# Optimization experiments

Measured on AMD Instinct MI355X. Metric: run time of the kernel, lower is better.

Reference implementation:

```python
import jax, jax.numpy as jnp
import numpy as np

B, C, H, W = 32, 256, 64, 64
K = 32

def setup_inputs() -> dict:
    key = jax.random.key(0)
    k1, k2, k3 = jax.random.split(key, 3)
    x = jax.random.normal(k1, (B, C, H, W), dtype=jnp.float32)
    codewords = jax.random.normal(k2, (K, C), dtype=jnp.float32)
    scale = jax.random.normal(k3, (K,), dtype=jnp.float32)
    return {"x": x, "codewords": codewords, "scale": scale}

def reference(x, codewords, scale):
    Bb, Cc, Hh, Ww = x.shape
    # features: [B, N, C] with N = H*W
    features = x.reshape(Bb, Cc, Hh * Ww).transpose(0, 2, 1)
    # Euclidean cdist via ||f||^2 + ||c||^2 - 2 f.c  -> [B, N, K]
    f2 = jnp.sum(features * features, axis=-1, keepdims=True)       # [B,N,1]
    c2 = jnp.sum(codewords * codewords, axis=-1)                     # [K]
    fc = jnp.einsum('bnc,kc->bnk', features, codewords)              # [B,N,K]
    dist = jnp.sqrt(jnp.maximum(f2 + c2[None, None, :] - 2.0 * fc, 0.0))
    # softmax over codewords with per-code scale
    assignment = jax.nn.softmax(-dist * scale[None, None, :], axis=2)  # [B,N,K]
    # encoded[b,k,c] = sum_n a[b,n,k] * (f[b,n,c] - cw[k,c])
    # factored to avoid materializing the [B,N,K,C] residual tensor
    enc = jnp.einsum('bnk,bnc->bkc', assignment, features)
    a_sum = jnp.sum(assignment, axis=1)                              # [B,K]
    encoded = enc - a_sum[:, :, None] * codewords[None, :, :]        # [B,K,C]
    return encoded.mean(axis=1)                                      # [B,C]
```

## Files before the change

### kernel.cpp

```cpp
#include <hip/hip_runtime.h>
#include <hip/hip_bf16.h>
#include <math.h>

#define B_DIM 32
#define C_DIM 256
#define K_DIM 32
#define N_DIM 4096
#define NSLICE 16
#define RS 66

typedef short v8s __attribute__((ext_vector_type(8)));
typedef float v4f __attribute__((ext_vector_type(4)));

#define WS_SPART 0
#define WS_APART 131072

__device__ __forceinline__ unsigned pack_bf16(float lo, float hi) {
    union { __hip_bfloat16 h; unsigned short u; } a, b;
    a.h = __float2bfloat16(lo);
    b.h = __float2bfloat16(hi);
    return ((unsigned)b.u << 16) | a.u;
}

__global__ __launch_bounds__(256, 2)
void ce_main(const float* __restrict__ x,
             const float* __restrict__ cw,
             const float* __restrict__ scale,
             float* __restrict__ Spart,
             float* __restrict__ a_part) {
    __shared__ float buf[2][4][16 * RS];
    __shared__ unsigned cwl[K_DIM][132];
    __shared__ float sA[4][C_DIM];
    __shared__ float awv[4][K_DIM];
    __shared__ float f2s[4][64];
    __shared__ float csl[64];

    const int tid   = threadIdx.x;
    const int wave  = tid >> 6;
    const int lane  = tid & 63;
    const int g     = lane >> 4;
    const int m     = lane & 15;
    const int ig    = lane >> 4;
    const int q     = lane & 15;
    const int slice = blockIdx.x;
    const int b     = blockIdx.y;

    const float* xw = x + (size_t)b * C_DIM * N_DIM + slice * 256 + wave * 64;

    float4 xv[8];
    #pragma unroll
    for (int j = 0; j < 4; ++j)
        #pragma unroll
        for (int r = 0; r < 2; ++r)
            xv[2 * j + r] = *(const float4*)(xw + (size_t)(2 * (4 * ig + j) + r) * N_DIM + 4 * q);

    {
        const int r = tid >> 3, c8 = tid & 7;
        float4 cv[8];
        #pragma unroll
        for (int j = 0; j < 8; ++j)
            cv[j] = ((const float4*)(cw + (size_t)r * C_DIM + c8 * 32))[j];
        float sq = 0.f;
        #pragma unroll
        for (int j = 0; j < 8; ++j) {
            sq = fmaf(cv[j].x, cv[j].x, sq);
            sq = fmaf(cv[j].y, cv[j].y, sq);
            sq = fmaf(cv[j].z, cv[j].z, sq);
            sq = fmaf(cv[j].w, cv[j].w, sq);
        }
        sq += __shfl_xor(sq, 1);
        sq += __shfl_xor(sq, 2);
        sq += __shfl_xor(sq, 4);
        if (c8 == 0) csl[r] = sq;
        if (tid < K_DIM) csl[32 + tid] = scale[tid];
        #pragma unroll
        for (int w = 0; w < 4; ++w) {
            uint4 o;
            o.x = pack_bf16(cv[2 * w].x, cv[2 * w].y);
            o.y = pack_bf16(cv[2 * w].z, cv[2 * w].w);
            o.z = pack_bf16(cv[2 * w + 1].x, cv[2 * w + 1].y);
            o.w = pack_bf16(cv[2 * w + 1].z, cv[2 * w + 1].w);
            *(uint4*)&cwl[r][16 * c8 + 4 * w] = o;
        }
    }
    __syncthreads();

    uint4 afr[2][8];
    #pragma unroll
    for (int u = 0; u < 2; ++u)
        #pragma unroll
        for (int s = 0; s < 8; ++s)
            afr[u][s] = ((const uint4*)&cwl[16 * u + m][0])[4 * s + g];

    float* b0 = &buf[0][wave][0];
    float* b1 = &buf[1][wave][0];

    v4f acc[2][4];
    #pragma unroll
    for (int u = 0; u < 2; ++u)
        #pragma unroll
        for (int t = 0; t < 4; ++t) acc[u][t] = (v4f){0.f, 0.f, 0.f, 0.f};

    float f2q[4] = {0.f, 0.f, 0.f, 0.f};
    float sLo[8], sHi[8];

    #pragma unroll
    for (int j = 0; j < 4; ++j) {
        float4 r0 = xv[2 * j], r1 = xv[2 * j + 1];
        f2q[0] = fmaf(r0.x, r0.x, f2q[0]); f2q[0] = fmaf(r1.x, r1.x, f2q[0]);
        f2q[1] = fmaf(r0.y, r0.y, f2q[1]); f2q[1] = fmaf(r1.y, r1.y, f2q[1]);
        f2q[2] = fmaf(r0.z, r0.z, f2q[2]); f2q[2] = fmaf(r1.z, r1.z, f2q[2]);
        f2q[3] = fmaf(r0.w, r0.w, f2q[3]); f2q[3] = fmaf(r1.w, r1.w, f2q[3]);
        unsigned* dst = &((unsigned*)b0)[(4 * ig + j) * RS + 4 * q];
        dst[0] = pack_bf16(r0.x, r1.x);
        dst[1] = pack_bf16(r0.y, r1.y);
        dst[2] = pack_bf16(r0.z, r1.z);
        dst[3] = pack_bf16(r0.w, r1.w);
    }

    #pragma unroll
    for (int s = 0; s < 8; ++s) {
        float* cb = (s & 1) ? b1 : b0;
        float* nb = (s & 1) ? b0 : b1;

        if (s < 7) {
            #pragma unroll
            for (int j = 0; j < 4; ++j)
                #pragma unroll
                for (int r = 0; r < 2; ++r)
                    xv[2 * j + r] = *(const float4*)(xw +
                        (size_t)(32 * (s + 1) + 2 * (4 * ig + j) + r) * N_DIM + 4 * q);
        }

        #pragma unroll
        for (int t = 0; t < 4; ++t) {
            union { unsigned d[4]; v8s v; } fb;
            #pragma unroll
            for (int h = 0; h < 4; ++h)
                fb.d[h] = ((const unsigned*)cb)[(4 * g + h) * RS + 16 * t + m];
            union { uint4 u; v8s v; } a0, a1;
            a0.u = afr[0][s]; a1.u = afr[1][s];
            acc[0][t] = __builtin_amdgcn_mfma_f32_16x16x32_bf16(a0.v, fb.v, acc[0][t], 0, 0, 0);
            acc[1][t] = __builtin_amdgcn_mfma_f32_16x16x32_bf16(a1.v, fb.v, acc[1][t], 0, 0, 0);
        }

        {
            float aLo = 0.f, aHi = 0.f;
            #pragma unroll
            for (int qq = 0; qq < 8; ++qq) {
                uint2 w = ((const uint2*)cb)[33 * m + 8 * g + qq];
                aLo += __uint_as_float(w.x << 16) + __uint_as_float(w.y << 16);
                aHi += __uint_as_float(w.x & 0xffff0000u) + __uint_as_float(w.y & 0xffff0000u);
            }
            aLo += __shfl_xor(aLo, 16); aLo += __shfl_xor(aLo, 32);
            aHi += __shfl_xor(aHi, 16); aHi += __shfl_xor(aHi, 32);
            sLo[s] = aLo; sHi[s] = aHi;
        }

        if (s < 7) {
            #pragma unroll
            for (int j = 0; j < 4; ++j) {
                float4 r0 = xv[2 * j], r1 = xv[2 * j + 1];
                f2q[0] = fmaf(r0.x, r0.x, f2q[0]); f2q[0] = fmaf(r1.x, r1.x, f2q[0]);
                f2q[1] = fmaf(r0.y, r0.y, f2q[1]); f2q[1] = fmaf(r1.y, r1.y, f2q[1]);
                f2q[2] = fmaf(r0.z, r0.z, f2q[2]); f2q[2] = fmaf(r1.z, r1.z, f2q[2]);
                f2q[3] = fmaf(r0.w, r0.w, f2q[3]); f2q[3] = fmaf(r1.w, r1.w, f2q[3]);
                unsigned* dst = &((unsigned*)nb)[(4 * ig + j) * RS + 4 * q];
                dst[0] = pack_bf16(r0.x, r1.x);
                dst[1] = pack_bf16(r0.y, r1.y);
                dst[2] = pack_bf16(r0.z, r1.z);
                dst[3] = pack_bf16(r0.w, r1.w);
            }
        }
    }

    #pragma unroll
    for (int p = 0; p < 4; ++p) {
        f2q[p] += __shfl_xor(f2q[p], 16);
        f2q[p] += __shfl_xor(f2q[p], 32);
    }
    if (lane < 16) {
        f2s[wave][4 * q + 0] = f2q[0];
        f2s[wave][4 * q + 1] = f2q[1];
        f2s[wave][4 * q + 2] = f2q[2];
        f2s[wave][4 * q + 3] = f2q[3];
    }

    float c2v[2][4], scv[2][4];
    #pragma unroll
    for (int u = 0; u < 2; ++u)
        #pragma unroll
        for (int r = 0; r < 4; ++r) {
            int k = 16 * u + 4 * g + r;
            c2v[u][r] = csl[k];
            scv[u][r] = csl[32 + k];
        }

    float aacc[2][4] = {{0.f,0.f,0.f,0.f},{0.f,0.f,0.f,0.f}};
    #pragma unroll
    for (int t = 0; t < 4; ++t) {
        float f2t = f2s[wave][16 * t + m];
        float L[2][4];
        float mx = -1e30f;
        #pragma unroll
        for (int u = 0; u < 2; ++u)
            #pragma unroll
            for (int r = 0; r < 4; ++r) {
                float d2 = f2t + c2v[u][r] - 2.f * acc[u][t][r];
                float dist = sqrtf(fmaxf(d2, 0.f));
                float Lv = -dist * scv[u][r];
                L[u][r] = Lv;
                mx = fmaxf(mx, Lv);
            }
        mx = fmaxf(mx, __shfl_xor(mx, 16));
        mx = fmaxf(mx, __shfl_xor(mx, 32));
        float e[2][4], ss = 0.f;
        #pragma unroll
        for (int u = 0; u < 2; ++u)
            #pragma unroll
            for (int r = 0; r < 4; ++r) {
                e[u][r] = __expf(L[u][r] - mx);
                ss += e[u][r];
            }
        ss += __shfl_xor(ss, 16);
        ss += __shfl_xor(ss, 32);
        float inv = 1.f / ss;
        #pragma unroll
        for (int u = 0; u < 2; ++u)
            #pragma unroll
            for (int r = 0; r < 4; ++r)
                aacc[u][r] = fmaf(e[u][r], inv, aacc[u][r]);
    }

    #pragma unroll
    for (int u = 0; u < 2; ++u)
        #pragma unroll
        for (int r = 0; r < 4; ++r) {
            float v = aacc[u][r];
            v += __shfl_xor(v, 1);
            v += __shfl_xor(v, 2);
            v += __shfl_xor(v, 4);
            v += __shfl_xor(v, 8);
            if (m == 0) awv[wave][16 * u + 4 * g + r] = v;
        }

    if (g == 0) {
        #pragma unroll
        for (int s = 0; s < 8; ++s) {
            sA[wave][32 * s + 2 * m]     = sLo[s];
            sA[wave][32 * s + 2 * m + 1] = sHi[s];
        }
    }
    __syncthreads();

    float Ssum = sA[0][tid] + sA[1][tid] + sA[2][tid] + sA[3][tid];
    Spart[((size_t)b * NSLICE + slice) * C_DIM + tid] = Ssum;
    if (tid < K_DIM)
        a_part[((size_t)b * NSLICE + slice) * K_DIM + tid] =
            awv[0][tid] + awv[1][tid] + awv[2][tid] + awv[3][tid];
}

__global__ void ce_final(float* __restrict__ out,
                         const float* __restrict__ cw,
                         const float* __restrict__ Spart,
                         const float* __restrict__ a_part) {
    __shared__ float asum[K_DIM];
    const int b = blockIdx.x;
    const int c = threadIdx.x;

    if (c < K_DIM) {
        float a = 0.f;
        #pragma unroll
        for (int s = 0; s < NSLICE; ++s)
            a += a_part[((size_t)b * NSLICE + s) * K_DIM + c];
        asum[c] = a;
    }
    __syncthreads();

    float S = 0.f;
    #pragma unroll
    for (int s = 0; s < NSLICE; ++s)
        S += Spart[((size_t)b * NSLICE + s) * C_DIM + c];

    float acc2 = 0.f;
    #pragma unroll
    for (int k = 0; k < K_DIM; ++k)
        acc2 = fmaf(asum[k], cw[k * C_DIM + c], acc2);
    out[b * C_DIM + c] = (S - acc2) * (1.0f / (float)K_DIM);
}

extern "C" void kernel_launch(void* const* d_in, const int* in_sizes, int n_in,
                              void* d_out, int out_size, void* d_ws, size_t ws_size,
                              hipStream_t stream) {
    const float* x     = (const float*)d_in[0];
    const float* cw    = (const float*)d_in[1];
    const float* scale = (const float*)d_in[2];
    float* out = (float*)d_out;
    float* ws  = (float*)d_ws;

    dim3 grid(NSLICE, B_DIM);
    ce_main<<<grid, 256, 0, stream>>>(x, cw, scale,
                                      ws + WS_SPART, ws + WS_APART);

    ce_final<<<B_DIM, 256, 0, stream>>>(out, cw,
                                        ws + WS_SPART, ws + WS_APART);
}
```

Baseline: 40.65 us.

## Split each block's pixels across eight waves and compute channel sums in fp32

Doubles the threads per block from 256 to 512 so each wave handles 32 pixels instead of 64, which halves per-thread registers and global loads. Codeword MFMA fragments are now loaded from LDS on every step rather than held in registers for the whole loop. Per-channel sums are computed from the fp32 values during packing with shuffle reductions, replacing the separate pass that read the bf16 LDS tile back. The intent is more resident waves to hide memory latency, at the cost of more LDS traffic and more cross-wave reduction work.

```diff
diff --git a/kernel.cpp b/kernel.cpp
--- a/kernel.cpp
+++ b/kernel.cpp
@@ -7,7 +7,7 @@
 #define K_DIM 32
 #define N_DIM 4096
 #define NSLICE 16
-#define RS 66
+#define RSD 34
 
 typedef short v8s __attribute__((ext_vector_type(8)));
 typedef float v4f __attribute__((ext_vector_type(4)));
@@ -22,17 +22,17 @@
     return ((unsigned)b.u << 16) | a.u;
 }
 
-__global__ __launch_bounds__(256, 2)
+__global__ __launch_bounds__(512, 4)
 void ce_main(const float* __restrict__ x,
              const float* __restrict__ cw,
              const float* __restrict__ scale,
              float* __restrict__ Spart,
              float* __restrict__ a_part) {
-    __shared__ float buf[2][4][16 * RS];
+    __shared__ float buf[2][8][16 * RSD];
     __shared__ unsigned cwl[K_DIM][132];
-    __shared__ float sA[4][C_DIM];
-    __shared__ float awv[4][K_DIM];
-    __shared__ float f2s[4][64];
+    __shared__ float sA[8][C_DIM];
+    __shared__ float awv[8][K_DIM];
+    __shared__ float f2s[8][32];
     __shared__ float csl[64];
 
     const int tid   = threadIdx.x;
@@ -40,29 +40,29 @@
     const int lane  = tid & 63;
     const int g     = lane >> 4;
     const int m     = lane & 15;
-    const int ig    = lane >> 4;
-    const int q     = lane & 15;
+    const int r0    = lane >> 3;
+    const int qd    = lane & 7;
     const int slice = blockIdx.x;
     const int b     = blockIdx.y;
 
-    const float* xw = x + (size_t)b * C_DIM * N_DIM + slice * 256 + wave * 64;
-
-    float4 xv[8];
-    #pragma unroll
-    for (int j = 0; j < 4; ++j)
-        #pragma unroll
-        for (int r = 0; r < 2; ++r)
-            xv[2 * j + r] = *(const float4*)(xw + (size_t)(2 * (4 * ig + j) + r) * N_DIM + 4 * q);
+    const float* xw = x + (size_t)b * C_DIM * N_DIM + slice * 256 + wave * 32;
+
+    float4 xv[4];
+    #pragma unroll
+    for (int j = 0; j < 2; ++j)
+        #pragma unroll
+        for (int rr = 0; rr < 2; ++rr)
+            xv[2 * j + rr] = *(const float4*)(xw + (size_t)(2 * (r0 + 8 * j) + rr) * N_DIM + 4 * qd);
 
     {
-        const int r = tid >> 3, c8 = tid & 7;
-        float4 cv[8];
-        #pragma unroll
-        for (int j = 0; j < 8; ++j)
-            cv[j] = ((const float4*)(cw + (size_t)r * C_DIM + c8 * 32))[j];
+        const int r = tid >> 4, c16 = tid & 15;
+        float4 cv[4];
+        #pragma unroll
+        for (int j = 0; j < 4; ++j)
+            cv[j] = ((const float4*)(cw + (size_t)r * C_DIM + c16 * 16))[j];
         float sq = 0.f;
         #pragma unroll
-        for (int j = 0; j < 8; ++j) {
+        for (int j = 0; j < 4; ++j) {
             sq = fmaf(cv[j].x, cv[j].x, sq);
             sq = fmaf(cv[j].y, cv[j].y, sq);
             sq = fmaf(cv[j].z, cv[j].z, sq);
@@ -71,52 +71,63 @@
         sq += __shfl_xor(sq, 1);
         sq += __shfl_xor(sq, 2);
         sq += __shfl_xor(sq, 4);
-        if (c8 == 0) csl[r] = sq;
+        sq += __shfl_xor(sq, 8);
+        if (c16 == 0) csl[r] = sq;
         if (tid < K_DIM) csl[32 + tid] = scale[tid];
-        #pragma unroll
-        for (int w = 0; w < 4; ++w) {
-            uint4 o;
-            o.x = pack_bf16(cv[2 * w].x, cv[2 * w].y);
-            o.y = pack_bf16(cv[2 * w].z, cv[2 * w].w);
-            o.z = pack_bf16(cv[2 * w + 1].x, cv[2 * w + 1].y);
-            o.w = pack_bf16(cv[2 * w + 1].z, cv[2 * w + 1].w);
-            *(uint4*)&cwl[r][16 * c8 + 4 * w] = o;
-        }
+        uint4 o0, o1;
+        o0.x = pack_bf16(cv[0].x, cv[0].y); o0.y = pack_bf16(cv[0].z, cv[0].w);
+        o0.z = pack_bf16(cv[1].x, cv[1].y); o0.w = pack_bf16(cv[1].z, cv[1].w);
+        o1.x = pack_bf16(cv[2].x, cv[2].y); o1.y = pack_bf16(cv[2].z, cv[2].w);
+        o1.z = pack_bf16(cv[3].x, cv[3].y); o1.w = pack_bf16(cv[3].z, cv[3].w);
+        *(uint4*)&cwl[r][8 * c16]     = o0;
+        *(uint4*)&cwl[r][8 * c16 + 4] = o1;
     }
     __syncthreads();
-
-    uint4 afr[2][8];
-    #pragma unroll
-    for (int u = 0; u < 2; ++u)
-        #pragma unroll
-        for (int s = 0; s < 8; ++s)
-            afr[u][s] = ((const uint4*)&cwl[16 * u + m][0])[4 * s + g];
 
     float* b0 = &buf[0][wave][0];
     float* b1 = &buf[1][wave][0];
 
-    v4f acc[2][4];
+    v4f acc[2][2];
     #pragma unroll
     for (int u = 0; u < 2; ++u)
         #pragma unroll
-        for (int t = 0; t < 4; ++t) acc[u][t] = (v4f){0.f, 0.f, 0.f, 0.f};
+        for (int t = 0; t < 2; ++t) acc[u][t] = (v4f){0.f, 0.f, 0.f, 0.f};
 
     float f2q[4] = {0.f, 0.f, 0.f, 0.f};
-    float sLo[8], sHi[8];
-
-    #pragma unroll
-    for (int j = 0; j < 4; ++j) {
-        float4 r0 = xv[2 * j], r1 = xv[2 * j + 1];
-        f2q[0] = fmaf(r0.x, r0.x, f2q[0]); f2q[0] = fmaf(r1.x, r1.x, f2q[0]);
-        f2q[1] = fmaf(r0.y, r0.y, f2q[1]); f2q[1] = fmaf(r1.y, r1.y, f2q[1]);
-        f2q[2] = fmaf(r0.z, r0.z, f2q[2]); f2q[2] = fmaf(r1.z, r1.z, f2q[2]);
-        f2q[3] = fmaf(r0.w, r0.w, f2q[3]); f2q[3] = fmaf(r1.w, r1.w, f2q[3]);
-        unsigned* dst = &((unsigned*)b0)[(4 * ig + j) * RS + 4 * q];
-        dst[0] = pack_bf16(r0.x, r1.x);
-        dst[1] = pack_bf16(r0.y, r1.y);
-        dst[2] = pack_bf16(r0.z, r1.z);
-        dst[3] = pack_bf16(r0.w, r1.w);
-    }
+
+    auto PACK = [&](float* bp, int sp) {
+        unsigned* bu = (unsigned*)bp;
+        float s4[4];
+        #pragma unroll
+        for (int j = 0; j < 2; ++j) {
+            float4 ra = xv[2 * j], rb = xv[2 * j + 1];
+            f2q[0] = fmaf(ra.x, ra.x, f2q[0]); f2q[0] = fmaf(rb.x, rb.x, f2q[0]);
+            f2q[1] = fmaf(ra.y, ra.y, f2q[1]); f2q[1] = fmaf(rb.y, rb.y, f2q[1]);
+            f2q[2] = fmaf(ra.z, ra.z, f2q[2]); f2q[2] = fmaf(rb.z, rb.z, f2q[2]);
+            f2q[3] = fmaf(ra.w, ra.w, f2q[3]); f2q[3] = fmaf(rb.w, rb.w, f2q[3]);
+            s4[2 * j]     = (ra.x + ra.y) + (ra.z + ra.w);
+            s4[2 * j + 1] = (rb.x + rb.y) + (rb.z + rb.w);
+            unsigned* dst = &bu[(r0 + 8 * j) * RSD + 4 * qd];
+            dst[0] = pack_bf16(ra.x, rb.x);
+            dst[1] = pack_bf16(ra.y, rb.y);
+            dst[2] = pack_bf16(ra.z, rb.z);
+            dst[3] = pack_bf16(ra.w, rb.w);
+        }
+        #pragma unroll
+        for (int i = 0; i < 4; ++i) {
+            s4[i] += __shfl_xor(s4[i], 1);
+            s4[i] += __shfl_xor(s4[i], 2);
+            s4[i] += __shfl_xor(s4[i], 4);
+        }
+        if (qd == 0) {
+            sA[wave][32 * sp + 2 * r0]           = s4[0];
+            sA[wave][32 * sp + 2 * r0 + 1]       = s4[1];
+            sA[wave][32 * sp + 2 * (r0 + 8)]     = s4[2];
+            sA[wave][32 * sp + 2 * (r0 + 8) + 1] = s4[3];
+        }
+    };
+
+    PACK(b0, 0);
 
     #pragma unroll
     for (int s = 0; s < 8; ++s) {
@@ -125,65 +136,40 @@
 
         if (s < 7) {
             #pragma unroll
-            for (int j = 0; j < 4; ++j)
+            for (int j = 0; j < 2; ++j)
                 #pragma unroll
-                for (int r = 0; r < 2; ++r)
-                    xv[2 * j + r] = *(const float4*)(xw +
-                        (size_t)(32 * (s + 1) + 2 * (4 * ig + j) + r) * N_DIM + 4 * q);
-        }
-
-        #pragma unroll
-        for (int t = 0; t < 4; ++t) {
+                for (int rr = 0; rr < 2; ++rr)
+                    xv[2 * j + rr] = *(const float4*)(xw +
+                        (size_t)(32 * (s + 1) + 2 * (r0 + 8 * j) + rr) * N_DIM + 4 * qd);
+        }
+
+        union { uint4 u4; v8s v; } a0, a1;
+        a0.u4 = ((const uint4*)&cwl[m][0])[4 * s + g];
+        a1.u4 = ((const uint4*)&cwl[16 + m][0])[4 * s + g];
+        #pragma unroll
+        for (int t = 0; t < 2; ++t) {
             union { unsigned d[4]; v8s v; } fb;
             #pragma unroll
             for (int h = 0; h < 4; ++h)
-                fb.d[h] = ((const unsigned*)cb)[(4 * g + h) * RS + 16 * t + m];
-            union { uint4 u; v8s v; } a0, a1;
-            a0.u = afr[0][s]; a1.u = afr[1][s];
+                fb.d[h] = ((const unsigned*)cb)[(4 * g + h) * RSD + 16 * t + m];
             acc[0][t] = __builtin_amdgcn_mfma_f32_16x16x32_bf16(a0.v, fb.v, acc[0][t], 0, 0, 0);
             acc[1][t] = __builtin_amdgcn_mfma_f32_16x16x32_bf16(a1.v, fb.v, acc[1][t], 0, 0, 0);
         }
 
-        {
-            float aLo = 0.f, aHi = 0.f;
-            #pragma unroll
-            for (int qq = 0; qq < 8; ++qq) {
-                uint2 w = ((const uint2*)cb)[33 * m + 8 * g + qq];
-                aLo += __uint_as_float(w.x << 16) + __uint_as_float(w.y << 16);
-                aHi += __uint_as_float(w.x & 0xffff0000u) + __uint_as_float(w.y & 0xffff0000u);
-            }
-            aLo += __shfl_xor(aLo, 16); aLo += __shfl_xor(aLo, 32);
-            aHi += __shfl_xor(aHi, 16); aHi += __shfl_xor(aHi, 32);
-            sLo[s] = aLo; sHi[s] = aHi;
-        }
-
-        if (s < 7) {
-            #pragma unroll
-            for (int j = 0; j < 4; ++j) {
-                float4 r0 = xv[2 * j], r1 = xv[2 * j + 1];
-                f2q[0] = fmaf(r0.x, r0.x, f2q[0]); f2q[0] = fmaf(r1.x, r1.x, f2q[0]);
-                f2q[1] = fmaf(r0.y, r0.y, f2q[1]); f2q[1] = fmaf(r1.y, r1.y, f2q[1]);
-                f2q[2] = fmaf(r0.z, r0.z, f2q[2]); f2q[2] = fmaf(r1.z, r1.z, f2q[2]);
-                f2q[3] = fmaf(r0.w, r0.w, f2q[3]); f2q[3] = fmaf(r1.w, r1.w, f2q[3]);
-                unsigned* dst = &((unsigned*)nb)[(4 * ig + j) * RS + 4 * q];
-                dst[0] = pack_bf16(r0.x, r1.x);
-                dst[1] = pack_bf16(r0.y, r1.y);
-                dst[2] = pack_bf16(r0.z, r1.z);
-                dst[3] = pack_bf16(r0.w, r1.w);
-            }
-        }
+        if (s < 7) PACK(nb, s + 1);
     }
 
     #pragma unroll
     for (int p = 0; p < 4; ++p) {
+        f2q[p] += __shfl_xor(f2q[p], 8);
         f2q[p] += __shfl_xor(f2q[p], 16);
         f2q[p] += __shfl_xor(f2q[p], 32);
     }
-    if (lane < 16) {
-        f2s[wave][4 * q + 0] = f2q[0];
-        f2s[wave][4 * q + 1] = f2q[1];
-        f2s[wave][4 * q + 2] = f2q[2];
-        f2s[wave][4 * q + 3] = f2q[3];
+    if (lane < 8) {
+        f2s[wave][4 * qd + 0] = f2q[0];
+        f2s[wave][4 * qd + 1] = f2q[1];
+        f2s[wave][4 * qd + 2] = f2q[2];
+        f2s[wave][4 * qd + 3] = f2q[3];
     }
 
     float c2v[2][4], scv[2][4];
@@ -198,7 +184,7 @@
 
     float aacc[2][4] = {{0.f,0.f,0.f,0.f},{0.f,0.f,0.f,0.f}};
     #pragma unroll
-    for (int t = 0; t < 4; ++t) {
+    for (int t = 0; t < 2; ++t) {
         float f2t = f2s[wave][16 * t + m];
         float L[2][4];
         float mx = -1e30f;
@@ -243,21 +229,21 @@
             v += __shfl_xor(v, 8);
             if (m == 0) awv[wave][16 * u + 4 * g + r] = v;
         }
-
-    if (g == 0) {
-        #pragma unroll
-        for (int s = 0; s < 8; ++s) {
-            sA[wave][32 * s + 2 * m]     = sLo[s];
-            sA[wave][32 * s + 2 * m + 1] = sHi[s];
-        }
-    }
     __syncthreads();
 
-    float Ssum = sA[0][tid] + sA[1][tid] + sA[2][tid] + sA[3][tid];
-    Spart[((size_t)b * NSLICE + slice) * C_DIM + tid] = Ssum;
-    if (tid < K_DIM)
-        a_part[((size_t)b * NSLICE + slice) * K_DIM + tid] =
-            awv[0][tid] + awv[1][tid] + awv[2][tid] + awv[3][tid];
+    if (tid < C_DIM) {
+        float Ssum = 0.f;
+        #pragma unroll
+        for (int w = 0; w < 8; ++w) Ssum += sA[w][tid];
+        Spart[((size_t)b * NSLICE + slice) * C_DIM + tid] = Ssum;
+    }
+    if (tid >= C_DIM && tid < C_DIM + K_DIM) {
+        const int k = tid - C_DIM;
+        float asum = 0.f;
+        #pragma unroll
+        for (int w = 0; w < 8; ++w) asum += awv[w][k];
+        a_part[((size_t)b * NSLICE + slice) * K_DIM + k] = asum;
+    }
 }
 
 __global__ void ce_final(float* __restrict__ out,
@@ -299,7 +285,7 @@
     float* ws  = (float*)d_ws;
 
     dim3 grid(NSLICE, B_DIM);
-    ce_main<<<grid, 256, 0, stream>>>(x, cw, scale,
+    ce_main<<<grid, 512, 0, stream>>>(x, cw, scale,
                                       ws + WS_SPART, ws + WS_APART);
 
     ce_final<<<B_DIM, 256, 0, stream>>>(out, cw,
```

New measurement: 54.33 us. +33.6%, slower.
